# Kernel tuning notes

Measured on AMD Instinct MI355X. Metric: run time of the kernel, lower is better.

## Reference

```python
import jax, jax.numpy as jnp
import numpy as np

WIN = 9  # local window size per spatial dim

def _boxfilter3d(x):
    k = jnp.ones((1, 1, WIN, WIN, WIN), x.dtype) / float(WIN ** 3)
    return jax.lax.conv_general_dilated(
        x, k, window_strides=(1, 1, 1), padding='SAME',
        dimension_numbers=('NCDHW', 'OIDHW', 'NCDHW'))

def setup_inputs() -> dict:
    key = jax.random.key(0)
    k1, k2 = jax.random.split(key)
    shape = (2, 1, 160, 192, 160)
    y_true = jax.random.uniform(k1, shape, dtype=jnp.float32)
    y_pred = jax.random.uniform(k2, shape, dtype=jnp.float32)
    return {"y_true": y_true, "y_pred": y_pred}

def reference(y_true, y_pred):
    Ii, Ji = y_true, y_pred
    mu1 = _boxfilter3d(Ii)
    mu2 = _boxfilter3d(Ji)
    sigma1_sq = _boxfilter3d(Ii * Ii) - mu1 * mu1
    sigma2_sq = _boxfilter3d(Ji * Ji) - mu2 * mu2
    sigma12 = _boxfilter3d(Ii * Ji) - mu1 * mu2
    cc = (sigma12 * sigma12) / (sigma1_sq * sigma2_sq + 1e-5)
    return -jnp.mean(cc)
```

## Files before the change

kernel.cpp:

```cpp
#include <hip/hip_runtime.h>

#define DD 160
#define HH 192
#define WW 160
#define HWs (HH * WW)
#define NTOT 9830400.0f
#define DOUT 10
#define NIT  18
#define NBLK 1920

#define SDRS 62
#define SDP  1492
#define HSRS 10
#define HSC  162
#define HSP  810

typedef float    v4 __attribute__((ext_vector_type(4)));
typedef _Float16 h4 __attribute__((ext_vector_type(4)));
typedef _Float16 h2 __attribute__((ext_vector_type(2)));
typedef _Float16 h8 __attribute__((ext_vector_type(8)));

__device__ __forceinline__ void block_sync_lds() {
    __builtin_amdgcn_s_waitcnt(0xc07f);
    __builtin_amdgcn_s_barrier();
}
__device__ __forceinline__ v4 up(h4 x) { return __builtin_convertvector(x, v4); }
__device__ __forceinline__ h4 dnp(v4 x) {
    h2 a = __builtin_bit_cast(h2, __builtin_amdgcn_cvt_pkrtz(x[0], x[1]));
    h2 b = __builtin_bit_cast(h2, __builtin_amdgcn_cvt_pkrtz(x[2], x[3]));
    return __builtin_shufflevector(a, b, 0, 1, 2, 3);
}

__global__ __launch_bounds__(256, 3) void kf(const float* __restrict__ I,
                                             const float* __restrict__ J,
                                             float* __restrict__ partial) {
    __shared__ __align__(16) h4 SDL[2 * SDP];
    __shared__ __align__(16) v4 HSL[2 * HSP];
    __shared__ float red[256];

    const int tid = threadIdx.x;
    const int wgid = blockIdx.x;
    const int tl = (wgid & 7) * 240 + (wgid >> 3);
    const int bx = tl % 60, by = (tl / 60) % 16, b = tl / 960;
    const int w0 = (bx % 5) * 32, h0 = (bx / 5) * 16;
    const int d0 = by * DOUT;
    const int bid = tl;

    const int rt = tid ^ ((bx & 1) << 7);

    const bool p1 = rt < 240;
    const int r = rt / 10, g = rt % 10;
    const int gh = h0 - 4 + r, gw = w0 - 4 + g * 4;
    const bool colOK = p1 && gh >= 0 && gh < HH && gw >= 0 && gw < WW;
    const size_t colOff = (size_t)gh * WW + gw;
    const float* Ib = I + (size_t)b * DD * HWs + colOff;
    const float* Jb = J + (size_t)b * DD * HWs + colOff;
    const int sdwOff = r * SDRS + (r >> 3) * 2 + 6 * g;

    const bool p2 = rt < 100;
    const int g2 = rt % 10, ch2 = (rt / 10) % 5, hh0 = (rt / 50) * 8;
    const int sdrOff = hh0 * SDRS + (hh0 >> 3) * 2 + 6 * g2 +
                       (ch2 == 4 ? 4 + (g2 & 1) : ch2);
    const int hswOff = ch2 * HSC + hh0 * HSRS + g2;

    const bool p3 = rt >= 128;
    const int q3 = rt & 127;
    const int hh = q3 >> 3, sg = q3 & 7;
    const int hsrOff = hh * HSRS + sg;

    v4 sd0 = 0.f, sd1 = 0.f, sd2 = 0.f, sd3 = 0.f, sd4 = 0.f;
    v4 pLI = 0.f, pLJ = 0.f;
    v4 pOI = 0.f, pOJ = 0.f;
    float acc = 0.f;
    const float inv = 1.0f / 729.0f;

    {
        const int si = d0 - 4;
        if (colOK && si >= 0) {
            pLI = *(const v4*)(Ib + (size_t)si * HWs);
            pLJ = *(const v4*)(Jb + (size_t)si * HWs);
        }
    }

#pragma unroll
    for (int t = 0; t < NIT + 2; ++t) {
        if (t < NIT && p1) {
            const v4 cI = pLI, cJ = pLJ;
            v4 dI = cI, dJv = cJ;
            v4 dII = cI * cI, dJJ = cJ * cJ, dIJ = cI * cJ;
            if (t >= 9) {
                dI  -= pOI;        dJv -= pOJ;
                dII -= pOI * pOI;  dJJ -= pOJ * pOJ;  dIJ -= pOI * pOJ;
            }
            sd0 += dI; sd1 += dJv; sd2 += dII; sd3 += dJJ; sd4 += dIJ;
            h4* const qb = &SDL[(t & 1) * SDP + sdwOff];
            h4 c0 = dnp(sd0), c1 = dnp(sd1), c2 = dnp(sd2), c3 = dnp(sd3);
            *(h8*)qb       = __builtin_shufflevector(c0, c1, 0,1,2,3,4,5,6,7);
            *(h8*)(qb + 2) = __builtin_shufflevector(c2, c3, 0,1,2,3,4,5,6,7);
            qb[4 + (g & 1)] = dnp(sd4);
            pLI = 0.f; pLJ = 0.f;
            const int sn = d0 - 3 + t;
            if (t + 1 < NIT && colOK && sn >= 0 && sn < DD) {
                pLI = *(const v4*)(Ib + (size_t)sn * HWs);
                pLJ = *(const v4*)(Jb + (size_t)sn * HWs);
            }
            pOI = 0.f; pOJ = 0.f;
            const int so = d0 - 12 + t;
            if (t >= 8 && t + 1 < NIT && colOK && so >= 0) {
                pOI = *(const v4*)(Ib + (size_t)so * HWs);
                pOJ = *(const v4*)(Jb + (size_t)so * HWs);
            }
        }

        if (t >= 1 && t <= NIT && p2) {
            const int par = (t - 1) & 1;
            const h4* const sdr = &SDL[par * SDP + sdrOff];
            v4* const hsw = &HSL[par * HSP + hswOff];
            h4 s = sdr[0];
#pragma unroll
            for (int k = 1; k < 9; ++k)
                s += sdr[k * SDRS + (k >= 8 ? 2 : 0)];
            hsw[0] = up(s);
#pragma unroll
            for (int j = 1; j < 8; ++j) {
                s += sdr[(j + 8) * SDRS + 2] - sdr[(j - 1) * SDRS];
                hsw[j * HSRS] = up(s);
            }
        }

        if (t >= 10 && p3) {
            const v4* const hsr = &HSL[(t & 1) * HSP + hsrOff];
            float w[5][4];
#pragma unroll
            for (int c = 0; c < 5; ++c) {
                v4 fa = hsr[c * HSC];
                v4 fb = hsr[c * HSC + 1];
                v4 fc = hsr[c * HSC + 2];
                float s = fa[0] + fa[1] + fa[2] + fa[3] +
                          fb[0] + fb[1] + fb[2] + fb[3] + fc[0];
                w[c][0] = s;
                s += fc[1] - fa[0]; w[c][1] = s;
                s += fc[2] - fa[1]; w[c][2] = s;
                s += fc[3] - fa[2]; w[c][3] = s;
            }
#pragma unroll
            for (int e = 0; e < 4; ++e) {
                float mu1 = w[0][e] * inv, mu2 = w[1][e] * inv;
                float g1  = fmaf(-mu1, mu1, w[2][e] * inv);
                float g2v = fmaf(-mu2, mu2, w[3][e] * inv);
                float g12 = fmaf(-mu1, mu2, w[4][e] * inv);
                acc += __fdividef(g12 * g12, fmaf(g1, g2v, 1e-5f));
            }
        }

        block_sync_lds();
    }

    red[tid] = acc;
    __syncthreads();
    if (tid < 128) red[tid] += red[tid + 128];
    __syncthreads();
    if (tid < 64) {
        float a = red[tid] + red[tid + 64];
#pragma unroll
        for (int off = 32; off > 0; off >>= 1) a += __shfl_down(a, off);
        if (tid == 0) partial[bid] = a;
    }
}

__global__ void k3_final(const float* __restrict__ partial,
                         float* __restrict__ out) {
    __shared__ float r[1024];
    const int i = threadIdx.x;
    float v = (i < NBLK) ? partial[i] : 0.f;
    if (i + 1024 < NBLK) v += partial[i + 1024];
    r[i] = v;
    __syncthreads();
    for (int off = 512; off > 0; off >>= 1) {
        if (i < off) r[i] += r[i + off];
        __syncthreads();
    }
    if (i == 0) out[0] = -r[0] * (1.0f / NTOT);
}

extern "C" void kernel_launch(void* const* d_in, const int* in_sizes, int n_in,
                              void* d_out, int out_size, void* d_ws, size_t ws_size,
                              hipStream_t stream) {
    (void)in_sizes; (void)n_in; (void)out_size; (void)ws_size;
    const float* I = (const float*)d_in[0];
    const float* J = (const float*)d_in[1];
    float* out     = (float*)d_out;
    float* partial = (float*)d_ws;

    kf<<<dim3(NBLK), 256, 0, stream>>>(I, J, partial);
    k3_final<<<1, 1024, 0, stream>>>(partial, out);
}
```

Measured before the change: 150.7 us.

## Double depth per block, store H-sums in fp16, and raise occupancy

Each block now produces 20 output depth slices instead of 10, which halves the block count and cuts the redundant 8-slice halo loads and warm-up iterations per output. The H-direction partial sums are kept in LDS as fp16 instead of fp32, halving that buffer's footprint, which allows launch bounds of four blocks per CU. The sliding H-window now reuses earlier loads held in registers instead of re-reading them from LDS. The risks are extra fp16 rounding in the accumulated sums, more register pressure, and fewer blocks to balance across CUs.

```diff
diff --git a/kernel.cpp b/kernel.cpp
--- a/kernel.cpp
+++ b/kernel.cpp
@@ -5,9 +5,9 @@
 #define WW 160
 #define HWs (HH * WW)
 #define NTOT 9830400.0f
-#define DOUT 10
-#define NIT  18
-#define NBLK 1920
+#define DOUT 20
+#define NIT  28
+#define NBLK 960
 
 #define SDRS 62
 #define SDP  1492
@@ -31,17 +31,17 @@
     return __builtin_shufflevector(a, b, 0, 1, 2, 3);
 }
 
-__global__ __launch_bounds__(256, 3) void kf(const float* __restrict__ I,
+__global__ __launch_bounds__(256, 4) void kf(const float* __restrict__ I,
                                              const float* __restrict__ J,
                                              float* __restrict__ partial) {
     __shared__ __align__(16) h4 SDL[2 * SDP];
-    __shared__ __align__(16) v4 HSL[2 * HSP];
+    __shared__ __align__(16) h4 HSL[2 * HSP];
     __shared__ float red[256];
 
     const int tid = threadIdx.x;
     const int wgid = blockIdx.x;
-    const int tl = (wgid & 7) * 240 + (wgid >> 3);
-    const int bx = tl % 60, by = (tl / 60) % 16, b = tl / 960;
+    const int tl = (wgid & 7) * 120 + (wgid >> 3);
+    const int bx = tl % 60, by = (tl / 60) % 8, b = tl / 480;
     const int w0 = (bx % 5) * 32, h0 = (bx / 5) * 16;
     const int d0 = by * DOUT;
     const int bid = tl;
@@ -115,27 +115,32 @@
         if (t >= 1 && t <= NIT && p2) {
             const int par = (t - 1) & 1;
             const h4* const sdr = &SDL[par * SDP + sdrOff];
-            v4* const hsw = &HSL[par * HSP + hswOff];
+            h4* const hsw = &HSL[par * HSP + hswOff];
+            h4 keep[7];
             h4 s = sdr[0];
-#pragma unroll
-            for (int k = 1; k < 9; ++k)
-                s += sdr[k * SDRS + (k >= 8 ? 2 : 0)];
-            hsw[0] = up(s);
+            keep[0] = s;
+#pragma unroll
+            for (int k = 1; k < 9; ++k) {
+                h4 v = sdr[k * SDRS + (k >= 8 ? 2 : 0)];
+                if (k < 7) keep[k] = v;
+                s += v;
+            }
+            hsw[0] = s;
 #pragma unroll
             for (int j = 1; j < 8; ++j) {
-                s += sdr[(j + 8) * SDRS + 2] - sdr[(j - 1) * SDRS];
-                hsw[j * HSRS] = up(s);
+                s += sdr[(j + 8) * SDRS + 2] - keep[j - 1];
+                hsw[j * HSRS] = s;
             }
         }
 
         if (t >= 10 && p3) {
-            const v4* const hsr = &HSL[(t & 1) * HSP + hsrOff];
+            const h4* const hsr = &HSL[(t & 1) * HSP + hsrOff];
             float w[5][4];
 #pragma unroll
             for (int c = 0; c < 5; ++c) {
-                v4 fa = hsr[c * HSC];
-                v4 fb = hsr[c * HSC + 1];
-                v4 fc = hsr[c * HSC + 2];
+                v4 fa = up(hsr[c * HSC]);
+                v4 fb = up(hsr[c * HSC + 1]);
+                v4 fc = up(hsr[c * HSC + 2]);
                 float s = fa[0] + fa[1] + fa[2] + fa[3] +
                           fb[0] + fb[1] + fb[2] + fb[3] + fc[0];
                 w[c][0] = s;
@@ -172,9 +177,7 @@
                          float* __restrict__ out) {
     __shared__ float r[1024];
     const int i = threadIdx.x;
-    float v = (i < NBLK) ? partial[i] : 0.f;
-    if (i + 1024 < NBLK) v += partial[i + 1024];
-    r[i] = v;
+    r[i] = (i < NBLK) ? partial[i] : 0.f;
     __syncthreads();
     for (int off = 512; off > 0; off >>= 1) {
         if (i < off) r[i] += r[i + off];
```

Measured after the change: 141.5 us. 6.1% less time.
